# Kernel tuning notes

Hardware: AMD Instinct MI355X
Metric: run time of the kernel (lower is better)

The kernel has to match this reference:

```python
import jax, jax.numpy as jnp
import numpy as np

H = 4       # num_heads (forced == num_gates by reshape math in source)
G = 4       # num_gates
HID = 1024  # hidden_size
D = HID // H  # head_dim = 256
T = 512     # sequence length
B = 16      # batch


def setup_inputs() -> dict:
    key = jax.random.key(0)
    k1, k2, k3 = jax.random.split(key, 3)
    lim = 1.0 / np.sqrt(HID)
    # x holds pre-projected gate preactivations Wx: [T, B, 4*hidden]
    x = jax.random.normal(k1, (T, B, G * HID), dtype=jnp.float32) * 0.1
    recurrent_kernel = jax.random.uniform(k2, (H, D, G, D), dtype=jnp.float32, minval=-lim, maxval=lim)
    bias = jax.random.uniform(k3, (H, G, D), dtype=jnp.float32, minval=-lim, maxval=lim)
    return {"x": x, "recurrent_kernel": recurrent_kernel, "bias": bias}


def reference(x, recurrent_kernel, bias):
    # Reproduce the source's reshape chain (valid since H == G == 4):
    # rk: [H, D, G, D] -> permute(0,2,3,1) -> [H, G, D, D] -> reshape(H, D, H*D)
    rk1 = jnp.transpose(recurrent_kernel, (0, 2, 3, 1)).reshape(H, D, H * D)
    # transpose(1,2) -> [H, H*D, D] -> reshape(H, D, G*D)
    rk2 = jnp.swapaxes(rk1, 1, 2).reshape(H, D, G * D)
    bflat = bias.reshape(-1)  # head-major flatten, as in source
    Bsz = x.shape[1]
    zero = jnp.zeros((Bsz, HID), dtype=x.dtype)

    def step(carry, Wx_t):
        h, c, n, m = carry
        # Ry: [B,H,1,D] @ [1,H,D,G*D] -> [B,H,G*D] -> [B,H,G,D] -> [B,G,H,D] -> [B, G*HID]
        Ry = jnp.einsum('bhd,hdg->bhg', h.reshape(Bsz, H, D), rk2)
        Ry = Ry.reshape(Bsz, H, G, D).transpose(0, 2, 1, 3).reshape(Bsz, -1)
        raw = (Wx_t + Ry + bflat).reshape(Bsz, G, HID)
        iraw, fraw, zraw, oraw = raw[:, 0], raw[:, 1], raw[:, 2], raw[:, 3]
        logfplusm = m + jax.nn.log_sigmoid(fraw)
        # source: if all(n == 0): mnew = iraw else max(iraw, logfplusm)
        mnew = jnp.where(jnp.all(n == 0.0), iraw, jnp.maximum(iraw, logfplusm))
        ogate = jax.nn.sigmoid(oraw)
        igate = jnp.exp(iraw - mnew)
        fgate = jnp.exp(logfplusm - mnew)
        cnew = fgate * c + igate * jnp.tanh(zraw)
        nnew = fgate * h + igate  # faithful to source (uses hidden_state, not n)
        hnew = ogate * cnew / nnew
        return (hnew, cnew, nnew, mnew), hnew

    carry0 = (zero, zero, zero, zero)
    (hT, cT, nT, mT), outs = jax.lax.scan(step, carry0, x)
    # output = all_states[0][1:] (hidden over time), state = all_states[:, -1]
    final_state = jnp.stack((hT, cT, nT, mT), axis=0)
    return outs, final_state
```

## Files before the change

### kernel.cpp

```cpp
#include <hip/hip_runtime.h>
#include <hip/hip_fp16.h>
#include <stdint.h>


#define NTS 512
#define OUTS_ELEMS (NTS * 16 * 1024)

typedef _Float16 half2v __attribute__((ext_vector_type(2)));

__device__ __forceinline__ float fdot2f(uint32_t a, uint32_t b, float c) {
#if __has_builtin(__builtin_amdgcn_fdot2)
  union U { uint32_t u; half2v h; };
  U ua, ub; ua.u = a; ub.u = b;
  return __builtin_amdgcn_fdot2(ua.h, ub.h, c, false);
#else
  __half2 ha, hb;
  *(uint32_t*)&ha = a; *(uint32_t*)&hb = b;
  float2 fa = __half22float2(ha), fb = __half22float2(hb);
  return fmaf(fa.y, fb.y, fmaf(fa.x, fb.x, c));
#endif
}

__global__ void repack_weights(const float* __restrict__ rk,
                               uint32_t* __restrict__ wp) {
  int tid = blockIdx.x * 256 + threadIdx.x;
  int dd   = tid & 3;
  int lane = (tid >> 2) & 63;
  int m    = (tid >> 8) & 31;
  int w    = (tid >> 13) & 3;
  int hq   = tid >> 15;
  int head = hq >> 2, q4 = hq & 3;
  int j_local = lane & 15, kq = lane >> 4;
  int n = m * 4 + dd;
  int g = n >> 5, p = n & 31;
  int dlo = w * 16 + j_local;
  uint32_t word = 0;
  #pragma unroll
  for (int e = 0; e < 2; ++e) {
    int klo = 2 * p + e;
    int d1 = klo * 4 + g;
    int d2 = dlo * 4 + kq;
    float v = rk[head * 262144 + d1 * 1024 + q4 * 256 + d2];
    word |= (uint32_t)__half_as_ushort(__float2half(v)) << (16 * e);
  }
  wp[tid] = word;
}

__global__ __launch_bounds__(256) void slstm_main(
    const float* __restrict__ x, const float* __restrict__ bias,
    const uint32_t* __restrict__ wp, uint32_t* hex,
    float* __restrict__ out) {
  __shared__ __align__(16) unsigned short lh[2][256];

  const int bid = blockIdx.x;
  const int xcd = bid & 7, yy = bid >> 3;
  const int q4 = yy & 3, ii = yy >> 2;
  const int cc = xcd * 8 + ii;
  const int b = cc >> 2, head = cc & 3;
  const int lane = threadIdx.x & 63, w = threadIdx.x >> 6;
  const int j_local = lane & 15, kq = lane >> 4;
  const int j_abs = q4 * 64 + w * 16 + j_local;
  const int hq = head * 4 + q4;

  uint32_t wr_[128];
  {
    const uint4* wp4 = (const uint4*)wp;
    int base = ((hq * 4 + w) * 32) * 64 + lane;
    #pragma unroll
    for (int mm = 0; mm < 32; ++mm) {
      uint4 v = wp4[base + mm * 64];
      wr_[mm * 4 + 0] = v.x; wr_[mm * 4 + 1] = v.y;
      wr_[mm * 4 + 2] = v.z; wr_[mm * 4 + 3] = v.w;
    }
  }

  float bg[4];
  #pragma unroll
  for (int g = 0; g < 4; ++g) bg[g] = bias[g * 1024 + head * 256 + j_abs];

  const int xoff0 = b * 4096 + head * 256 + j_abs;
  float xv[4];
  #pragma unroll
  for (int g = 0; g < 4; ++g) xv[g] = x[xoff0 + g * 1024];

  const int rd_idx = cc * 256 + w * 64 + lane;
  const int wr_idx = cc * 256 + j_abs;
  const int out_off = b * 1024 + head * 256 + j_abs;

  float hs = 0.f, cs = 0.f, nns = 0.f, ms = 0.f;

  #pragma unroll 1
  for (int t = 0; t < NTS; ++t) {
    float a0 = 0.f, a1 = 0.f, a2 = 0.f, a3 = 0.f;
    if (t > 0) {
      const uint32_t tg = (uint32_t)(t - 1);
      uint32_t* sp = hex + ((t - 1) & 1) * 16384 + rd_idx;
      uint32_t v; int spins = 0;
      for (;;) {
        v = __hip_atomic_load(sp, __ATOMIC_RELAXED, __HIP_MEMORY_SCOPE_AGENT);
        if (__all((v & 0xffffu) == tg) || ++spins > (1 << 14)) break;
      }
      lh[t & 1][w * 64 + lane] = (unsigned short)(v >> 16);
      __syncthreads();
      uint32_t hr[32];
      {
        const float4* hp = (const float4*)&lh[t & 1][kq * 64];
        #pragma unroll
        for (int f = 0; f < 8; ++f) {
          float4 fv = hp[f];
          hr[f * 4 + 0] = __float_as_uint(fv.x);
          hr[f * 4 + 1] = __float_as_uint(fv.y);
          hr[f * 4 + 2] = __float_as_uint(fv.z);
          hr[f * 4 + 3] = __float_as_uint(fv.w);
        }
      }
      #pragma unroll
      for (int p = 0; p < 32; ++p) {
        uint32_t hh = hr[p];
        a0 = fdot2f(wr_[p],      hh, a0);
        a1 = fdot2f(wr_[32 + p], hh, a1);
        a2 = fdot2f(wr_[64 + p], hh, a2);
        a3 = fdot2f(wr_[96 + p], hh, a3);
      }
      a0 += __shfl_xor(a0, 16, 64); a0 += __shfl_xor(a0, 32, 64);
      a1 += __shfl_xor(a1, 16, 64); a1 += __shfl_xor(a1, 32, 64);
      a2 += __shfl_xor(a2, 16, 64); a2 += __shfl_xor(a2, 32, 64);
      a3 += __shfl_xor(a3, 16, 64); a3 += __shfl_xor(a3, 32, 64);
    }

    float ri = a0 + xv[0] + bg[0];
    float rf = a1 + xv[1] + bg[1];
    float rz = a2 + xv[2] + bg[2];
    float ro = a3 + xv[3] + bg[3];

    float xn0 = 0.f, xn1 = 0.f, xn2 = 0.f, xn3 = 0.f;
    if (t < NTS - 1) {
      int xo = xoff0 + (t + 1) * 65536;
      xn0 = x[xo]; xn1 = x[xo + 1024]; xn2 = x[xo + 2048]; xn3 = x[xo + 3072];
    }

    float lsf = fminf(rf, 0.f) - log1pf(__expf(-fabsf(rf)));
    float lf = ms + lsf;
    float mnew = (t == 0) ? ri : fmaxf(ri, lf);
    float og = 1.f / (1.f + __expf(-ro));
    float ig = __expf(ri - mnew);
    float fg = __expf(lf - mnew);
    float cnew = fg * cs + ig * tanhf(rz);
    float nnew = fg * hs + ig;
    float hnew = og * cnew / nnew;
    hs = hnew; cs = cnew; nns = nnew; ms = mnew;

    if (kq == 0) {
      out[t * 16384 + out_off] = hnew;
      uint32_t wword =
          ((uint32_t)__half_as_ushort(__float2half(hnew)) << 16) | (uint32_t)t;
      __hip_atomic_store(hex + (t & 1) * 16384 + wr_idx, wword,
                         __ATOMIC_RELAXED, __HIP_MEMORY_SCOPE_AGENT);
    }
    if (t < NTS - 1) { xv[0] = xn0; xv[1] = xn1; xv[2] = xn2; xv[3] = xn3; }
  }

  if (kq == 0) {
    float* fs = out + OUTS_ELEMS;
    int o = b * 1024 + head * 256 + j_abs;
    fs[o] = hs;
    fs[16384 + o] = cs;
    fs[32768 + o] = nns;
    fs[49152 + o] = ms;
  }
}

extern "C" void kernel_launch(void* const* d_in, const int* in_sizes, int n_in,
                              void* d_out, int out_size, void* d_ws,
                              size_t ws_size, hipStream_t stream) {
  const float* x    = (const float*)d_in[0];
  const float* rk   = (const float*)d_in[1];
  const float* bias = (const float*)d_in[2];
  uint32_t* wp  = (uint32_t*)d_ws;
  uint32_t* hex = (uint32_t*)((char*)d_ws + (1u << 21));
  float* out = (float*)d_out;

  repack_weights<<<2048, 256, 0, stream>>>(rk, wp);
  slstm_main<<<256, 256, 0, stream>>>(x, bias, wp, hex, out);
}
```

Baseline: 965.8 us.

## Split recurrent matvec by K-chunk per wave with LDS partial-sum reduction

Changes the work split inside each block so that each wave covers one 64-wide chunk of the hidden input for all 64 outputs, instead of a 16-output slice with cross-lane shuffle reductions. Partial sums go through LDS and are summed by the publishing wave and the owning wave. The owning wave writes its own h chunk straight to LDS rather than polling global memory, which takes one remote read off the critical path. The cost is an extra LDS round trip and reduction per step, plus gate math done redundantly in two waves.

```diff
diff --git a/kernel.cpp b/kernel.cpp
--- a/kernel.cpp
+++ b/kernel.cpp
@@ -30,27 +30,24 @@
   int w    = (tid >> 13) & 3;
   int hq   = tid >> 15;
   int head = hq >> 2, q4 = hq & 3;
-  int j_local = lane & 15, kq = lane >> 4;
   int n = m * 4 + dd;
   int g = n >> 5, p = n & 31;
-  int dlo = w * 16 + j_local;
   uint32_t word = 0;
   #pragma unroll
   for (int e = 0; e < 2; ++e) {
     int klo = 2 * p + e;
-    int d1 = klo * 4 + g;
-    int d2 = dlo * 4 + kq;
-    float v = rk[head * 262144 + d1 * 1024 + q4 * 256 + d2];
+    float v = rk[head * 262144 + (klo * 4 + g) * 1024 + q4 * 256 + lane * 4 + w];
     word |= (uint32_t)__half_as_ushort(__float2half(v)) << (16 * e);
   }
   wp[tid] = word;
 }
 
-__global__ __launch_bounds__(256) void slstm_main(
+__global__ __launch_bounds__(256, 1) void slstm_main(
     const float* __restrict__ x, const float* __restrict__ bias,
     const uint32_t* __restrict__ wp, uint32_t* hex,
     float* __restrict__ out) {
-  __shared__ __align__(16) unsigned short lh[2][256];
+  __shared__ __align__(16) unsigned short lh[4][64];
+  __shared__ __align__(16) float4 pa[2][4][64];
 
   const int bid = blockIdx.x;
   const int xcd = bid & 7, yy = bid >> 3;
@@ -58,9 +55,11 @@
   const int cc = xcd * 8 + ii;
   const int b = cc >> 2, head = cc & 3;
   const int lane = threadIdx.x & 63, w = threadIdx.x >> 6;
-  const int j_local = lane & 15, kq = lane >> 4;
-  const int j_abs = q4 * 64 + w * 16 + j_local;
   const int hq = head * 4 + q4;
+  const int j_abs = q4 * 64 + lane;
+  const bool is_pub = (w == 0);
+  const bool is_own = (w == q4);
+  const bool needs_gates = is_pub || is_own;
 
   uint32_t wr_[128];
   {
@@ -79,9 +78,11 @@
   for (int g = 0; g < 4; ++g) bg[g] = bias[g * 1024 + head * 256 + j_abs];
 
   const int xoff0 = b * 4096 + head * 256 + j_abs;
-  float xv[4];
-  #pragma unroll
-  for (int g = 0; g < 4; ++g) xv[g] = x[xoff0 + g * 1024];
+  float xv[4] = {0.f, 0.f, 0.f, 0.f};
+  if (needs_gates) {
+    #pragma unroll
+    for (int g = 0; g < 4; ++g) xv[g] = x[xoff0 + g * 1024];
+  }
 
   const int rd_idx = cc * 256 + w * 64 + lane;
   const int wr_idx = cc * 256 + j_abs;
@@ -91,20 +92,27 @@
 
   #pragma unroll 1
   for (int t = 0; t < NTS; ++t) {
-    float a0 = 0.f, a1 = 0.f, a2 = 0.f, a3 = 0.f;
+    float A0 = 0.f, A1 = 0.f, A2 = 0.f, A3 = 0.f;
+    float xn0 = 0.f, xn1 = 0.f, xn2 = 0.f, xn3 = 0.f;
     if (t > 0) {
-      const uint32_t tg = (uint32_t)(t - 1);
-      uint32_t* sp = hex + ((t - 1) & 1) * 16384 + rd_idx;
-      uint32_t v; int spins = 0;
-      for (;;) {
-        v = __hip_atomic_load(sp, __ATOMIC_RELAXED, __HIP_MEMORY_SCOPE_AGENT);
-        if (__all((v & 0xffffu) == tg) || ++spins > (1 << 14)) break;
-      }
-      lh[t & 1][w * 64 + lane] = (unsigned short)(v >> 16);
-      __syncthreads();
-      uint32_t hr[32];
+      if (!is_own) {
+        const uint32_t tg = (uint32_t)(t - 1);
+        uint32_t* sp = hex + ((t - 1) & 1) * 16384 + rd_idx;
+        uint32_t v; int spins = 0;
+        for (;;) {
+          v = __hip_atomic_load(sp, __ATOMIC_RELAXED, __HIP_MEMORY_SCOPE_AGENT);
+          if (__all((v & 0xffffu) == tg) || ++spins > (1 << 15)) break;
+        }
+        lh[w][lane] = (unsigned short)(v >> 16);
+      }
+      if (needs_gates && t < NTS - 1) {
+        int xo = xoff0 + (t + 1) * 65536;
+        xn0 = x[xo]; xn1 = x[xo + 1024]; xn2 = x[xo + 2048]; xn3 = x[xo + 3072];
+      }
+      float a0 = 0.f, a1 = 0.f, a2 = 0.f, a3 = 0.f;
       {
-        const float4* hp = (const float4*)&lh[t & 1][kq * 64];
+        uint32_t hr[32];
+        const float4* hp = (const float4*)&lh[w][0];
         #pragma unroll
         for (int f = 0; f < 8; ++f) {
           float4 fv = hp[f];
@@ -113,60 +121,68 @@
           hr[f * 4 + 2] = __float_as_uint(fv.z);
           hr[f * 4 + 3] = __float_as_uint(fv.w);
         }
-      }
-      #pragma unroll
-      for (int p = 0; p < 32; ++p) {
-        uint32_t hh = hr[p];
-        a0 = fdot2f(wr_[p],      hh, a0);
-        a1 = fdot2f(wr_[32 + p], hh, a1);
-        a2 = fdot2f(wr_[64 + p], hh, a2);
-        a3 = fdot2f(wr_[96 + p], hh, a3);
-      }
-      a0 += __shfl_xor(a0, 16, 64); a0 += __shfl_xor(a0, 32, 64);
-      a1 += __shfl_xor(a1, 16, 64); a1 += __shfl_xor(a1, 32, 64);
-      a2 += __shfl_xor(a2, 16, 64); a2 += __shfl_xor(a2, 32, 64);
-      a3 += __shfl_xor(a3, 16, 64); a3 += __shfl_xor(a3, 32, 64);
+        #pragma unroll
+        for (int p = 0; p < 32; ++p) {
+          uint32_t hh = hr[p];
+          a0 = fdot2f(wr_[p],      hh, a0);
+          a1 = fdot2f(wr_[32 + p], hh, a1);
+          a2 = fdot2f(wr_[64 + p], hh, a2);
+          a3 = fdot2f(wr_[96 + p], hh, a3);
+        }
+      }
+      pa[t & 1][w][lane] = make_float4(a0, a1, a2, a3);
+      __syncthreads();
+      if (needs_gates) {
+        #pragma unroll
+        for (int ww = 0; ww < 4; ++ww) {
+          float4 pv = pa[t & 1][ww][lane];
+          A0 += pv.x; A1 += pv.y; A2 += pv.z; A3 += pv.w;
+        }
+      }
+    } else {
+      if (needs_gates) {
+        int xo = xoff0 + 65536;
+        xn0 = x[xo]; xn1 = x[xo + 1024]; xn2 = x[xo + 2048]; xn3 = x[xo + 3072];
+      }
     }
 
-    float ri = a0 + xv[0] + bg[0];
-    float rf = a1 + xv[1] + bg[1];
-    float rz = a2 + xv[2] + bg[2];
-    float ro = a3 + xv[3] + bg[3];
-
-    float xn0 = 0.f, xn1 = 0.f, xn2 = 0.f, xn3 = 0.f;
-    if (t < NTS - 1) {
-      int xo = xoff0 + (t + 1) * 65536;
-      xn0 = x[xo]; xn1 = x[xo + 1024]; xn2 = x[xo + 2048]; xn3 = x[xo + 3072];
+    if (needs_gates) {
+      float ri = A0 + xv[0] + bg[0];
+      float rf = A1 + xv[1] + bg[1];
+      float rz = A2 + xv[2] + bg[2];
+      float ro = A3 + xv[3] + bg[3];
+
+      float lsf = fminf(rf, 0.f) - log1pf(__expf(-fabsf(rf)));
+      float lf = ms + lsf;
+      float mnew = (t == 0) ? ri : fmaxf(ri, lf);
+      float og = 1.f / (1.f + __expf(-ro));
+      float ig = __expf(ri - mnew);
+      float fg = __expf(lf - mnew);
+      float cnew = fg * cs + ig * tanhf(rz);
+      float nnew = fg * hs + ig;
+      float hnew = og * cnew / nnew;
+      hs = hnew; cs = cnew; nns = nnew; ms = mnew;
+
+      unsigned short hf = __half_as_ushort(__float2half(hnew));
+      if (is_pub) {
+        out[t * 16384 + out_off] = hnew;
+        uint32_t wword = ((uint32_t)hf << 16) | (uint32_t)t;
+        __hip_atomic_store(hex + (t & 1) * 16384 + wr_idx, wword,
+                           __ATOMIC_RELAXED, __HIP_MEMORY_SCOPE_AGENT);
+      }
+      if (is_own) {
+        lh[w][lane] = hf;
+      }
+      xv[0] = xn0; xv[1] = xn1; xv[2] = xn2; xv[3] = xn3;
     }
-
-    float lsf = fminf(rf, 0.f) - log1pf(__expf(-fabsf(rf)));
-    float lf = ms + lsf;
-    float mnew = (t == 0) ? ri : fmaxf(ri, lf);
-    float og = 1.f / (1.f + __expf(-ro));
-    float ig = __expf(ri - mnew);
-    float fg = __expf(lf - mnew);
-    float cnew = fg * cs + ig * tanhf(rz);
-    float nnew = fg * hs + ig;
-    float hnew = og * cnew / nnew;
-    hs = hnew; cs = cnew; nns = nnew; ms = mnew;
-
-    if (kq == 0) {
-      out[t * 16384 + out_off] = hnew;
-      uint32_t wword =
-          ((uint32_t)__half_as_ushort(__float2half(hnew)) << 16) | (uint32_t)t;
-      __hip_atomic_store(hex + (t & 1) * 16384 + wr_idx, wword,
-                         __ATOMIC_RELAXED, __HIP_MEMORY_SCOPE_AGENT);
-    }
-    if (t < NTS - 1) { xv[0] = xn0; xv[1] = xn1; xv[2] = xn2; xv[3] = xn3; }
-  }
-
-  if (kq == 0) {
+  }
+
+  if (is_pub) {
     float* fs = out + OUTS_ELEMS;
-    int o = b * 1024 + head * 256 + j_abs;
-    fs[o] = hs;
-    fs[16384 + o] = cs;
-    fs[32768 + o] = nns;
-    fs[49152 + o] = ms;
+    fs[out_off] = hs;
+    fs[16384 + out_off] = cs;
+    fs[32768 + out_off] = nns;
+    fs[49152 + out_off] = ms;
   }
 }
 
```

After: 933.2 us. 1.03x faster.

## Batch recurrent matvec across batch with MFMA and repartition to 16 blocks

Applied to the files above, without the earlier changes.

Replaces the per-(batch,head) fdot2 matvec with MFMA 16x16x32 f16 tiles that process all 16 batch rows at once. The grid shrinks to 16 active blocks, each owning one head and a 64-column slice. Blocks exchange hidden-state slices through the global flag-tagged buffer, and each block keeps its own slice in LDS. Fast exp-based tanh and log replace the library calls. Fewer blocks each take on more per-step work, and every step now crosses two __syncthreads plus a wider cross-block spin.

```diff
diff --git a/kernel.cpp b/kernel.cpp
--- a/kernel.cpp
+++ b/kernel.cpp
@@ -6,167 +6,194 @@
 #define NTS 512
 #define OUTS_ELEMS (NTS * 16 * 1024)
 
-typedef _Float16 half2v __attribute__((ext_vector_type(2)));
-
-__device__ __forceinline__ float fdot2f(uint32_t a, uint32_t b, float c) {
-#if __has_builtin(__builtin_amdgcn_fdot2)
-  union U { uint32_t u; half2v h; };
-  U ua, ub; ua.u = a; ub.u = b;
-  return __builtin_amdgcn_fdot2(ua.h, ub.h, c, false);
-#else
-  __half2 ha, hb;
-  *(uint32_t*)&ha = a; *(uint32_t*)&hb = b;
-  float2 fa = __half22float2(ha), fb = __half22float2(hb);
-  return fmaf(fa.y, fb.y, fmaf(fa.x, fb.x, c));
-#endif
-}
+typedef _Float16 v8h __attribute__((ext_vector_type(8)));
+typedef float v4f __attribute__((ext_vector_type(4)));
+
+union F16x8 { uint32_t u[4]; v8h h; };
 
 __global__ void repack_weights(const float* __restrict__ rk,
                                uint32_t* __restrict__ wp) {
   int tid = blockIdx.x * 256 + threadIdx.x;
-  int dd   = tid & 3;
+  int c    = tid & 3;
   int lane = (tid >> 2) & 63;
-  int m    = (tid >> 8) & 31;
-  int w    = (tid >> 13) & 3;
-  int hq   = tid >> 15;
-  int head = hq >> 2, q4 = hq & 3;
-  int j_local = lane & 15, kq = lane >> 4;
-  int n = m * 4 + dd;
-  int g = n >> 5, p = n & 31;
-  int dlo = w * 16 + j_local;
+  int kk   = (tid >> 8) & 7;
+  int nt   = (tid >> 11) & 3;
+  int g    = (tid >> 13) & 3;
+  int jq   = (tid >> 15) & 3;
+  int head = tid >> 17;
+  int dout = jq * 64 + nt * 16 + (lane & 15);
   uint32_t word = 0;
   #pragma unroll
   for (int e = 0; e < 2; ++e) {
-    int klo = 2 * p + e;
-    int d1 = klo * 4 + g;
-    int d2 = dlo * 4 + kq;
-    float v = rk[head * 262144 + d1 * 1024 + q4 * 256 + d2];
+    int din = kk * 32 + (lane >> 4) * 8 + c * 2 + e;
+    float v = rk[head * 262144 + ((din & 63) * 4 + g) * 1024 + jq * 256 +
+                 (dout & 63) * 4 + (din >> 6)];
     word |= (uint32_t)__half_as_ushort(__float2half(v)) << (16 * e);
   }
   wp[tid] = word;
 }
 
-__global__ __launch_bounds__(256) void slstm_main(
+__global__ __launch_bounds__(256, 1) void slstm_main(
     const float* __restrict__ x, const float* __restrict__ bias,
     const uint32_t* __restrict__ wp, uint32_t* hex,
     float* __restrict__ out) {
-  __shared__ __align__(16) unsigned short lh[2][256];
-
   const int bid = blockIdx.x;
-  const int xcd = bid & 7, yy = bid >> 3;
-  const int q4 = yy & 3, ii = yy >> 2;
-  const int cc = xcd * 8 + ii;
-  const int b = cc >> 2, head = cc & 3;
-  const int lane = threadIdx.x & 63, w = threadIdx.x >> 6;
-  const int j_local = lane & 15, kq = lane >> 4;
-  const int j_abs = q4 * 64 + w * 16 + j_local;
-  const int hq = head * 4 + q4;
-
-  uint32_t wr_[128];
+  const int head = bid & 7;
+  const int jq = bid >> 3;
+  if (head >= 4) return;
+
+  const int lane = threadIdx.x & 63;
+  const int w = threadIdx.x >> 6;
+  const int m15 = lane & 15, quad = lane >> 4;
+
+  __shared__ __align__(16) unsigned short h_lds[16][264];
+  __shared__ float raw_lds[4][16][66];
+
+  uint32_t bw[128];
   {
     const uint4* wp4 = (const uint4*)wp;
-    int base = ((hq * 4 + w) * 32) * 64 + lane;
-    #pragma unroll
-    for (int mm = 0; mm < 32; ++mm) {
-      uint4 v = wp4[base + mm * 64];
-      wr_[mm * 4 + 0] = v.x; wr_[mm * 4 + 1] = v.y;
-      wr_[mm * 4 + 2] = v.z; wr_[mm * 4 + 3] = v.w;
-    }
-  }
-
+    #pragma unroll
+    for (int nt = 0; nt < 4; ++nt)
+      #pragma unroll
+      for (int kk = 0; kk < 8; ++kk) {
+        uint4 v = wp4[((((head * 4 + jq) * 4 + w) * 4 + nt) * 8 + kk) * 64 + lane];
+        int i = (nt * 8 + kk) * 4;
+        bw[i] = v.x; bw[i + 1] = v.y; bw[i + 2] = v.z; bw[i + 3] = v.w;
+      }
+    #pragma unroll
+    for (int i = 0; i < 128; ++i) asm volatile("" : "+v"(bw[i]));
+  }
+
+  const int xcol = head * 256 + jq * 64 + lane;
   float bg[4];
   #pragma unroll
-  for (int g = 0; g < 4; ++g) bg[g] = bias[g * 1024 + head * 256 + j_abs];
-
-  const int xoff0 = b * 4096 + head * 256 + j_abs;
-  float xv[4];
-  #pragma unroll
-  for (int g = 0; g < 4; ++g) xv[g] = x[xoff0 + g * 1024];
-
-  const int rd_idx = cc * 256 + w * 64 + lane;
-  const int wr_idx = cc * 256 + j_abs;
-  const int out_off = b * 1024 + head * 256 + j_abs;
-
-  float hs = 0.f, cs = 0.f, nns = 0.f, ms = 0.f;
+  for (int g = 0; g < 4; ++g) bg[g] = bias[g * 1024 + xcol];
+
+  float xv[16];
+  #pragma unroll
+  for (int r = 0; r < 4; ++r)
+    #pragma unroll
+    for (int g = 0; g < 4; ++g)
+      xv[r * 4 + g] = x[(w * 4 + r) * 4096 + g * 1024 + xcol];
+
+  float hs[4] = {0.f, 0.f, 0.f, 0.f}, cs[4] = {0.f, 0.f, 0.f, 0.f};
+  float nns[4] = {0.f, 0.f, 0.f, 0.f}, msx[4] = {0.f, 0.f, 0.f, 0.f};
 
   #pragma unroll 1
   for (int t = 0; t < NTS; ++t) {
-    float a0 = 0.f, a1 = 0.f, a2 = 0.f, a3 = 0.f;
     if (t > 0) {
       const uint32_t tg = (uint32_t)(t - 1);
-      uint32_t* sp = hex + ((t - 1) & 1) * 16384 + rd_idx;
-      uint32_t v; int spins = 0;
-      for (;;) {
-        v = __hip_atomic_load(sp, __ATOMIC_RELAXED, __HIP_MEMORY_SCOPE_AGENT);
-        if (__all((v & 0xffffu) == tg) || ++spins > (1 << 14)) break;
-      }
-      lh[t & 1][w * 64 + lane] = (unsigned short)(v >> 16);
-      __syncthreads();
-      uint32_t hr[32];
-      {
-        const float4* hp = (const float4*)&lh[t & 1][kq * 64];
-        #pragma unroll
-        for (int f = 0; f < 8; ++f) {
-          float4 fv = hp[f];
-          hr[f * 4 + 0] = __float_as_uint(fv.x);
-          hr[f * 4 + 1] = __float_as_uint(fv.y);
-          hr[f * 4 + 2] = __float_as_uint(fv.z);
-          hr[f * 4 + 3] = __float_as_uint(fv.w);
+      uint32_t* base = hex + ((t - 1) & 1) * 16384 + head * 4096;
+      uint32_t vv[4][4];
+      bool ok; int spins = 0;
+      do {
+        ok = true;
+        #pragma unroll
+        for (int s = 0; s < 4; ++s) {
+          if (s == jq) continue;
+          #pragma unroll
+          for (int r = 0; r < 4; ++r) {
+            uint32_t v = __hip_atomic_load(base + (w * 4 + r) * 256 + s * 64 + lane,
+                                           __ATOMIC_RELAXED,
+                                           __HIP_MEMORY_SCOPE_AGENT);
+            vv[s][r] = v;
+            ok = ok && ((v & 0xffffu) == tg);
+          }
         }
-      }
-      #pragma unroll
-      for (int p = 0; p < 32; ++p) {
-        uint32_t hh = hr[p];
-        a0 = fdot2f(wr_[p],      hh, a0);
-        a1 = fdot2f(wr_[32 + p], hh, a1);
-        a2 = fdot2f(wr_[64 + p], hh, a2);
-        a3 = fdot2f(wr_[96 + p], hh, a3);
-      }
-      a0 += __shfl_xor(a0, 16, 64); a0 += __shfl_xor(a0, 32, 64);
-      a1 += __shfl_xor(a1, 16, 64); a1 += __shfl_xor(a1, 32, 64);
-      a2 += __shfl_xor(a2, 16, 64); a2 += __shfl_xor(a2, 32, 64);
-      a3 += __shfl_xor(a3, 16, 64); a3 += __shfl_xor(a3, 32, 64);
-    }
-
-    float ri = a0 + xv[0] + bg[0];
-    float rf = a1 + xv[1] + bg[1];
-    float rz = a2 + xv[2] + bg[2];
-    float ro = a3 + xv[3] + bg[3];
-
-    float xn0 = 0.f, xn1 = 0.f, xn2 = 0.f, xn3 = 0.f;
+      } while (!__all(ok) && ++spins < (1 << 15));
+      #pragma unroll
+      for (int s = 0; s < 4; ++s) {
+        if (s == jq) continue;
+        #pragma unroll
+        for (int r = 0; r < 4; ++r)
+          h_lds[w * 4 + r][s * 64 + lane] = (unsigned short)(vv[s][r] >> 16);
+      }
+    }
+    __syncthreads();
+
+    if (t > 0) {
+      v4f acc[4];
+      #pragma unroll
+      for (int nt = 0; nt < 4; ++nt) acc[nt] = (v4f){0.f, 0.f, 0.f, 0.f};
+      #pragma unroll
+      for (int kk = 0; kk < 8; ++kk) {
+        F16x8 af;
+        uint4 a4 = *(const uint4*)&h_lds[m15][kk * 32 + quad * 8];
+        af.u[0] = a4.x; af.u[1] = a4.y; af.u[2] = a4.z; af.u[3] = a4.w;
+        #pragma unroll
+        for (int nt = 0; nt < 4; ++nt) {
+          F16x8 bf; int i = (nt * 8 + kk) * 4;
+          bf.u[0] = bw[i]; bf.u[1] = bw[i + 1];
+          bf.u[2] = bw[i + 2]; bf.u[3] = bw[i + 3];
+          acc[nt] = __builtin_amdgcn_mfma_f32_16x16x32_f16(af.h, bf.h, acc[nt],
+                                                           0, 0, 0);
+        }
+      }
+      #pragma unroll
+      for (int nt = 0; nt < 4; ++nt)
+        #pragma unroll
+        for (int r = 0; r < 4; ++r)
+          raw_lds[w][quad * 4 + r][nt * 16 + m15] = acc[nt][r];
+    }
+    __syncthreads();
+
+    float xn[16];
     if (t < NTS - 1) {
-      int xo = xoff0 + (t + 1) * 65536;
-      xn0 = x[xo]; xn1 = x[xo + 1024]; xn2 = x[xo + 2048]; xn3 = x[xo + 3072];
-    }
-
-    float lsf = fminf(rf, 0.f) - log1pf(__expf(-fabsf(rf)));
-    float lf = ms + lsf;
-    float mnew = (t == 0) ? ri : fmaxf(ri, lf);
-    float og = 1.f / (1.f + __expf(-ro));
-    float ig = __expf(ri - mnew);
-    float fg = __expf(lf - mnew);
-    float cnew = fg * cs + ig * tanhf(rz);
-    float nnew = fg * hs + ig;
-    float hnew = og * cnew / nnew;
-    hs = hnew; cs = cnew; nns = nnew; ms = mnew;
-
-    if (kq == 0) {
-      out[t * 16384 + out_off] = hnew;
-      uint32_t wword =
-          ((uint32_t)__half_as_ushort(__float2half(hnew)) << 16) | (uint32_t)t;
-      __hip_atomic_store(hex + (t & 1) * 16384 + wr_idx, wword,
+      #pragma unroll
+      for (int r = 0; r < 4; ++r)
+        #pragma unroll
+        for (int g = 0; g < 4; ++g)
+          xn[r * 4 + g] = x[(t + 1) * 65536 + (w * 4 + r) * 4096 + g * 1024 + xcol];
+    }
+    #pragma unroll
+    for (int r = 0; r < 4; ++r) {
+      float a0 = 0.f, a1 = 0.f, a2 = 0.f, a3 = 0.f;
+      if (t > 0) {
+        a0 = raw_lds[0][w * 4 + r][lane];
+        a1 = raw_lds[1][w * 4 + r][lane];
+        a2 = raw_lds[2][w * 4 + r][lane];
+        a3 = raw_lds[3][w * 4 + r][lane];
+      }
+      float ri = a0 + xv[r * 4 + 0] + bg[0];
+      float rf = a1 + xv[r * 4 + 1] + bg[1];
+      float rz = a2 + xv[r * 4 + 2] + bg[2];
+      float ro = a3 + xv[r * 4 + 3] + bg[3];
+
+      float lsf = fminf(rf, 0.f) - __logf(1.f + __expf(-fabsf(rf)));
+      float lf = msx[r] + lsf;
+      float mnew = (t == 0) ? ri : fmaxf(ri, lf);
+      float og = 1.f / (1.f + __expf(-ro));
+      float ig = __expf(ri - mnew);
+      float fg = __expf(lf - mnew);
+      float ez = __expf(2.f * rz);
+      float th = 1.f - 2.f / (ez + 1.f);
+      float cnew = fg * cs[r] + ig * th;
+      float nnew = fg * hs[r] + ig;
+      float hnew = og * cnew / nnew;
+      hs[r] = hnew; cs[r] = cnew; nns[r] = nnew; msx[r] = mnew;
+
+      out[t * 16384 + (w * 4 + r) * 1024 + xcol] = hnew;
+      unsigned short hf = __half_as_ushort(__float2half(hnew));
+      h_lds[w * 4 + r][jq * 64 + lane] = hf;
+      __hip_atomic_store(hex + (t & 1) * 16384 + head * 4096 +
+                             (w * 4 + r) * 256 + jq * 64 + lane,
+                         ((uint32_t)hf << 16) | (uint32_t)t,
                          __ATOMIC_RELAXED, __HIP_MEMORY_SCOPE_AGENT);
     }
-    if (t < NTS - 1) { xv[0] = xn0; xv[1] = xn1; xv[2] = xn2; xv[3] = xn3; }
-  }
-
-  if (kq == 0) {
-    float* fs = out + OUTS_ELEMS;
-    int o = b * 1024 + head * 256 + j_abs;
-    fs[o] = hs;
-    fs[16384 + o] = cs;
-    fs[32768 + o] = nns;
-    fs[49152 + o] = ms;
+    if (t < NTS - 1) {
+      #pragma unroll
+      for (int i = 0; i < 16; ++i) xv[i] = xn[i];
+    }
+  }
+
+  float* fs = out + OUTS_ELEMS;
+  #pragma unroll
+  for (int r = 0; r < 4; ++r) {
+    int o = (w * 4 + r) * 1024 + xcol;
+    fs[o] = hs[r];
+    fs[16384 + o] = cs[r];
+    fs[32768 + o] = nns[r];
+    fs[49152 + o] = msx[r];
   }
 }
 
@@ -181,5 +208,5 @@
   float* out = (float*)d_out;
 
   repack_weights<<<2048, 256, 0, stream>>>(rk, wp);
-  slstm_main<<<256, 256, 0, stream>>>(x, bias, wp, hex, out);
+  slstm_main<<<32, 256, 0, stream>>>(x, bias, wp, hex, out);
 }
```

Measured after the change: 1.933 ms. 2x slower.
